# Kernel optimization log

Hardware: AMD Instinct MI355X
Metric: run time of the kernel (lower is better)

The kernel has to match this reference:

```python
import jax, jax.numpy as jnp
from jax import lax
import numpy as np

VOCAB = 50000
E = 301  # 300-dim pretrained + appended ones column
D = 25
NUM_CLASSES = 5


def setup_inputs() -> dict:
    key = jax.random.key(0)
    ks = jax.random.split(key, 8)
    B, S = 2048, 128
    words = jax.random.randint(ks[0], (B, S), 0, VOCAB)
    emb = jax.random.normal(ks[1], (VOCAB, E - 1), dtype=jnp.float32)
    # hstack ones column as in __init__
    emb_table = jnp.concatenate([emb, jnp.ones((VOCAB, 1), jnp.float32)], axis=1)
    A = jax.random.normal(ks[2], (D, E, D), dtype=jnp.float32) * 0.02
    W = jax.random.normal(ks[3], (E, D), dtype=jnp.float32) * 0.02
    V = jax.random.normal(ks[4], (D, D), dtype=jnp.float32) * 0.02
    b = jax.random.normal(ks[5], (D,), dtype=jnp.float32) * 0.02
    out_W = jax.random.normal(ks[6], (NUM_CLASSES, D), dtype=jnp.float32) * 0.02
    out_b = jax.random.normal(ks[7], (NUM_CLASSES,), dtype=jnp.float32) * 0.02
    return {"words": words, "batch_size": B, "emb_table": emb_table,
            "A": A, "W": W, "V": V, "b": b, "out_W": out_W, "out_b": out_b}


def reference(words, batch_size, emb_table, A, W, V, b, out_W, out_b):
    x_seq = emb_table[words]                      # [B, S, E] frozen embedding gather
    h0 = jnp.zeros((batch_size, D), jnp.float32).at[:, -1].set(1.0)

    def step(h, x):  # x: [B, E], h: [B, D]
        # a[b,i] = sum_{e,j} x[b,e] A[i,e,j] h[b,j]  (bilinear tensor term)
        a = jnp.einsum('be,ied,bd->bi', x, A, h)
        lin = x @ W + h @ V + b
        return jnp.tanh(a + lin), None

    h, _ = lax.scan(step, h0, jnp.swapaxes(x_seq, 0, 1))  # scan over S
    logits = h @ out_W.T + out_b                 # [B, num_classes]
    return jax.nn.sigmoid(logits)
```

## Files before the change

kernel.cpp:

```cpp
#include <hip/hip_runtime.h>
#include <math.h>

#define VOCAB 50000
#define EE 301
#define KP 304
#define DD 25
#define SEQ 128
#define NC 5
#define BROW 768
#define NUSE 700
#define TROW 704
#define EMT 50048

#define GLOAD_LDS16(g, l) __builtin_amdgcn_global_load_lds( \
    (const __attribute__((address_space(1))) void*)(g),     \
    (__attribute__((address_space(3))) void*)(l), 16, 0, 0)

__global__ __launch_bounds__(256) void build_B(
    const float* __restrict__ A, const float* __restrict__ W,
    float* __restrict__ Bmat)
{
    int e = blockIdx.x;
    for (int c = threadIdx.x; c < BROW; c += 256) {
        float v = 0.f;
        if (e < EE && c < NUSE) {
            int i = c / 28, j = c % 28;
            if (j < 25)       v = A[((size_t)i * EE + e) * DD + j];
            else if (j == 25) v = W[(size_t)e * DD + i];
        }
        Bmat[(size_t)e * BROW + c] = v;
    }
}

__global__ __launch_bounds__(256) void transpose_emb(
    const float* __restrict__ emb, float* __restrict__ embT)
{
    __shared__ float t[64][65];
    int m0 = blockIdx.x * 64, k0 = blockIdx.y * 64;
    int tx = threadIdx.x & 63, ty = threadIdx.x >> 6;
#pragma unroll
    for (int it = 0; it < 16; ++it) {
        int m = m0 + ty * 16 + it;
        int k = k0 + tx;
        t[tx][ty * 16 + it] = (m < VOCAB && k < EE) ? emb[(size_t)m * EE + k] : 0.f;
    }
    __syncthreads();
#pragma unroll
    for (int it = 0; it < 16; ++it) {
        int kl = ty * 16 + it;
        int k = k0 + kl;
        if (k < KP) embT[(size_t)k * EMT + m0 + tx] = t[kl][tx];
    }
}

__global__ __launch_bounds__(256, 2) void gemm_T2(
    const float* __restrict__ embT,
    const float* __restrict__ Bmat,
    float* __restrict__ T)
{
    __shared__ float As[2][16][128];
    __shared__ float Bs[2][16][128];
    int tid = threadIdx.x;
    int tx = tid & 15, ty = tid >> 4;
    int m0 = blockIdx.x * 128, n0 = blockIdx.y * 128;
    int wave = tid >> 6, lane = tid & 63;
    int krow = lane >> 5;
    int col4 = (lane & 31) * 4;

    float acc[8][8];
#pragma unroll
    for (int a = 0; a < 8; ++a)
#pragma unroll
        for (int c = 0; c < 8; ++c) acc[a][c] = 0.f;

    auto dma_tile = [&](int k0, int buf) {
#pragma unroll
        for (int j = 0; j < 2; ++j) {
            int r0 = wave * 4 + j * 2;
            int k = k0 + r0 + krow;
            GLOAD_LDS16(embT + (size_t)k * EMT + m0 + col4, &As[buf][r0][0]);
            GLOAD_LDS16(Bmat + (size_t)k * BROW + n0 + col4, &Bs[buf][r0][0]);
        }
    };

    dma_tile(0, 0);
    __syncthreads();

    int buf = 0;
    for (int k0 = 0; k0 < KP; k0 += 16) {
        if (k0 + 16 < KP) dma_tile(k0 + 16, buf ^ 1);
#pragma unroll
        for (int kk = 0; kk < 16; ++kk) {
            float4 a0 = *(const float4*)&As[buf][kk][ty * 4];
            float4 a1 = *(const float4*)&As[buf][kk][64 + ty * 4];
            float4 b0 = *(const float4*)&Bs[buf][kk][tx * 4];
            float4 b1 = *(const float4*)&Bs[buf][kk][64 + tx * 4];
            float av[8] = {a0.x, a0.y, a0.z, a0.w, a1.x, a1.y, a1.z, a1.w};
            float bv[8] = {b0.x, b0.y, b0.z, b0.w, b1.x, b1.y, b1.z, b1.w};
#pragma unroll
            for (int a = 0; a < 8; ++a)
#pragma unroll
                for (int c = 0; c < 8; ++c)
                    acc[a][c] = fmaf(av[a], bv[c], acc[a][c]);
        }
        __syncthreads();
        buf ^= 1;
    }

#pragma unroll
    for (int gi = 0; gi < 2; ++gi) {
#pragma unroll
        for (int r = 0; r < 4; ++r) {
            int m = m0 + gi * 64 + ty * 4 + r;
            if (m < VOCAB) {
                float* row = T + (size_t)m * TROW;
#pragma unroll
                for (int gc = 0; gc < 2; ++gc) {
                    int n = n0 + gc * 64 + tx * 4;
                    if (n < TROW) {
                        int a = gi * 4 + r, c = gc * 4;
                        *(float4*)(row + n) = make_float4(
                            acc[a][c], acc[a][c + 1], acc[a][c + 2], acc[a][c + 3]);
                    }
                }
            }
        }
    }
}

__global__ __launch_bounds__(256, 2) void gemm_T(
    const float* __restrict__ emb, const float* __restrict__ Bmat,
    float* __restrict__ T)
{
    __shared__ float As[2][16][132];
    __shared__ float Bs[2][16][132];
    int tid = threadIdx.x;
    int tx = tid & 15, ty = tid >> 4;
    int m0 = blockIdx.x * 128, n0 = blockIdx.y * 128;
    float acc[8][8];
#pragma unroll
    for (int a = 0; a < 8; ++a)
#pragma unroll
        for (int c = 0; c < 8; ++c) acc[a][c] = 0.f;
    float ar[8]; float4 br[2];
    int kl0 = tid >> 5, nl0 = (tid & 31) * 4;
#pragma unroll
    for (int it = 0; it < 8; ++it) {
        int m = m0 + ty + 16 * it, k = tx;
        ar[it] = (m < VOCAB && k < EE) ? emb[(size_t)m * EE + k] : 0.f;
    }
#pragma unroll
    for (int it = 0; it < 2; ++it) {
        int k = kl0 + 8 * it;
        br[it] = (k < EE) ? *(const float4*)(Bmat + (size_t)k * BROW + n0 + nl0)
                          : make_float4(0.f, 0.f, 0.f, 0.f);
    }
#pragma unroll
    for (int it = 0; it < 8; ++it) As[0][tx][ty + 16 * it] = ar[it];
#pragma unroll
    for (int it = 0; it < 2; ++it) *(float4*)(&Bs[0][kl0 + 8 * it][nl0]) = br[it];
    __syncthreads();
    int buf = 0;
    for (int k0 = 0; k0 < EE; k0 += 16) {
        int k1 = k0 + 16;
        bool more = (k1 < EE);
        if (more) {
#pragma unroll
            for (int it = 0; it < 8; ++it) {
                int m = m0 + ty + 16 * it, k = k1 + tx;
                ar[it] = (m < VOCAB && k < EE) ? emb[(size_t)m * EE + k] : 0.f;
            }
#pragma unroll
            for (int it = 0; it < 2; ++it) {
                int k = k1 + kl0 + 8 * it;
                br[it] = (k < EE) ? *(const float4*)(Bmat + (size_t)k * BROW + n0 + nl0)
                                  : make_float4(0.f, 0.f, 0.f, 0.f);
            }
        }
#pragma unroll
        for (int kk = 0; kk < 16; ++kk) {
            float4 a0 = *(const float4*)&As[buf][kk][ty * 4];
            float4 a1 = *(const float4*)&As[buf][kk][64 + ty * 4];
            float4 b0 = *(const float4*)&Bs[buf][kk][tx * 4];
            float4 b1 = *(const float4*)&Bs[buf][kk][64 + tx * 4];
            float av[8] = {a0.x, a0.y, a0.z, a0.w, a1.x, a1.y, a1.z, a1.w};
            float bv[8] = {b0.x, b0.y, b0.z, b0.w, b1.x, b1.y, b1.z, b1.w};
#pragma unroll
            for (int a = 0; a < 8; ++a)
#pragma unroll
                for (int c = 0; c < 8; ++c)
                    acc[a][c] = fmaf(av[a], bv[c], acc[a][c]);
        }
        if (more) {
            int nb = buf ^ 1;
#pragma unroll
            for (int it = 0; it < 8; ++it) As[nb][tx][ty + 16 * it] = ar[it];
#pragma unroll
            for (int it = 0; it < 2; ++it) *(float4*)(&Bs[nb][kl0 + 8 * it][nl0]) = br[it];
            __syncthreads();
            buf = nb;
        }
    }
#pragma unroll
    for (int gi = 0; gi < 2; ++gi) {
#pragma unroll
        for (int r = 0; r < 4; ++r) {
            int m = m0 + gi * 64 + ty * 4 + r;
            if (m < VOCAB) {
                float* row = T + (size_t)m * TROW;
#pragma unroll
                for (int gc = 0; gc < 2; ++gc) {
                    int n = n0 + gc * 64 + tx * 4;
                    if (n < TROW) {
                        int a = gi * 4 + r, c = gc * 4;
                        *(float4*)(row + n) = make_float4(
                            acc[a][c], acc[a][c + 1], acc[a][c + 2], acc[a][c + 3]);
                    }
                }
            }
        }
    }
}

__global__ __launch_bounds__(256) void rnn_scan_np5(
    const int*   __restrict__ words,
    const float* __restrict__ T,
    const float* __restrict__ V,
    const float* __restrict__ bvec,
    const float* __restrict__ outW,
    const float* __restrict__ outB,
    float* __restrict__ out,
    int B)
{
    int tid = threadIdx.x;
    int g = tid >> 5, i = tid & 31;
    int b = blockIdx.x * 8 + g;
    bool act = (i < DD) && (b < B);
    int ii = (i < DD) ? i : (DD - 1);
    int bsafe = (b < B) ? b : 0;
    const int* wr = words + (size_t)bsafe * SEQ;

    float Vcol[DD];
#pragma unroll
    for (int j = 0; j < DD; ++j) Vcol[j] = V[j * DD + ii];
    float bi = bvec[ii];

    float hr[DD];
#pragma unroll
    for (int j = 0; j < DD; ++j) hr[j] = 0.f;
    hr[DD - 1] = 1.f;

    bool sse = ((b & 3) == 0) && ((i & 3) == 0);
    const float* base = T + (size_t)ii * 28;

    float4 A0[7], A1[7], A2[7];
    auto LD = [&](float4* dst, int t) {
        const float* R = base + (size_t)wr[t] * TROW;
#pragma unroll
        for (int u = 0; u < 7; ++u) dst[u] = *(const float4*)(R + u * 4);
    };

    float hnew = 0.f;
    auto STEP = [&](const float4* C) {
        float Tj[28];
#pragma unroll
        for (int u = 0; u < 7; ++u) {
            Tj[u * 4 + 0] = C[u].x; Tj[u * 4 + 1] = C[u].y;
            Tj[u * 4 + 2] = C[u].z; Tj[u * 4 + 3] = C[u].w;
        }
        float qv = Tj[25];
        float a;
        if (sse) {
            float p0 = 0.f, p1 = 0.f, p2 = 0.f, p3 = 0.f;
#pragma unroll
            for (int j = 0; j < 24; j += 4) {
                p0 = __fadd_rn(p0, __fmul_rn(Tj[j],     hr[j]));
                p1 = __fadd_rn(p1, __fmul_rn(Tj[j + 1], hr[j + 1]));
                p2 = __fadd_rn(p2, __fmul_rn(Tj[j + 2], hr[j + 2]));
                p3 = __fadd_rn(p3, __fmul_rn(Tj[j + 3], hr[j + 3]));
            }
            float s02 = __fadd_rn(p0, p2);
            float s13 = __fadd_rn(p1, p3);
            a = __fadd_rn(s02, s13);
            a = __fadd_rn(a, __fmul_rn(Tj[24], hr[24]));
        } else {
            a = 0.f;
#pragma unroll
            for (int j = 0; j < DD; ++j)
                a = __fadd_rn(a, __fmul_rn(Tj[j], hr[j]));
        }
        float r2 = 0.f;
#pragma unroll
        for (int j = 0; j < DD; ++j)
            r2 = fmaf(hr[j], Vcol[j], r2);
        float lin = __fadd_rn(__fadd_rn(qv, r2), bi);
        float pre = __fadd_rn(a, lin);
        hnew = act ? (float)tanh((double)pre) : 0.f;
#pragma unroll
        for (int j = 0; j < DD; ++j)
            hr[j] = __shfl(hnew, j, 32);
    };

    LD(A0, 0);
    LD(A1, 1);
    for (int t = 0; t + 2 < SEQ; t += 3) {
        LD(A2, t + 2); STEP(A0);
        LD(A0, t + 3); STEP(A1);
        LD(A1, t + 4); STEP(A2);
    }
    STEP(A0);
    STEP(A1);

    if (i < NC && b < B) {
        float acc = 0.f;
#pragma unroll
        for (int j = 0; j < DD; ++j)
            acc = fmaf(hr[j], outW[i * DD + j], acc);
        float l = __fadd_rn(acc, outB[i]);
        out[(size_t)b * NC + i] = (float)(1.0 / (1.0 + exp(-(double)l)));
    }
}

extern "C" void kernel_launch(void* const* d_in, const int* in_sizes, int n_in,
                              void* d_out, int out_size, void* d_ws, size_t ws_size,
                              hipStream_t stream)
{
    const int*   words = (const int*)d_in[0];
    const float* emb   = (const float*)d_in[2];
    const float* A     = (const float*)d_in[3];
    const float* W     = (const float*)d_in[4];
    const float* V     = (const float*)d_in[5];
    const float* bias  = (const float*)d_in[6];
    const float* outW  = (const float*)d_in[7];
    const float* outB  = (const float*)d_in[8];
    float* out = (float*)d_out;
    int B = in_sizes[0] / SEQ;

    const size_t T_OFF    = (size_t)1 << 20;
    const size_t EMBT_OFF = (size_t)144 << 20;
    const size_t NEED     = EMBT_OFF + (size_t)KP * EMT * 4;
    float* Bmat = (float*)d_ws;
    float* T    = (float*)((char*)d_ws + T_OFF);
    float* embT = (float*)((char*)d_ws + EMBT_OFF);

    build_B<<<KP, 256, 0, stream>>>(A, W, Bmat);
    if (ws_size >= NEED) {
        transpose_emb<<<dim3(EMT / 64, (KP + 63) / 64), 256, 0, stream>>>(emb, embT);
        gemm_T2<<<dim3((VOCAB + 127) / 128, 6), 256, 0, stream>>>(embT, Bmat, T);
    } else {
        gemm_T<<<dim3((VOCAB + 127) / 128, 6), 256, 0, stream>>>(emb, Bmat, T);
    }
    rnn_scan_np5<<<(B + 7) / 8, 256, 0, stream>>>(words, T, V, bias, outW, outB, out, B);
}
```

Measured before the change: 511.3 us.

## Widen GEMM tile to 128x256 and deepen scan prefetch to four steps

The precompute GEMM now gives each block a 128x256 output tile with 8x16 accumulators per thread, halving the grid in N and the number of times each embT row is re-read. Launch bounds drop to one block per SM to leave room for the extra registers. The RNN scan kernel now prefetches gathered T rows four steps ahead instead of three, to hide more gather latency. The cost is higher register pressure and lower occupancy in both kernels, and the N tiling now computes columns up to 768 that are discarded past 704.

```diff
diff --git a/kernel.cpp b/kernel.cpp
--- a/kernel.cpp
+++ b/kernel.cpp
@@ -53,25 +53,25 @@
     }
 }
 
-__global__ __launch_bounds__(256, 2) void gemm_T2(
+__global__ __launch_bounds__(256, 1) void gemm_T3(
     const float* __restrict__ embT,
     const float* __restrict__ Bmat,
     float* __restrict__ T)
 {
     __shared__ float As[2][16][128];
-    __shared__ float Bs[2][16][128];
+    __shared__ float Bs[2][16][256];
     int tid = threadIdx.x;
     int tx = tid & 15, ty = tid >> 4;
-    int m0 = blockIdx.x * 128, n0 = blockIdx.y * 128;
+    int m0 = blockIdx.x * 128, n0 = blockIdx.y * 256;
     int wave = tid >> 6, lane = tid & 63;
     int krow = lane >> 5;
     int col4 = (lane & 31) * 4;
 
-    float acc[8][8];
+    float acc[8][16];
 #pragma unroll
     for (int a = 0; a < 8; ++a)
 #pragma unroll
-        for (int c = 0; c < 8; ++c) acc[a][c] = 0.f;
+        for (int c = 0; c < 16; ++c) acc[a][c] = 0.f;
 
     auto dma_tile = [&](int k0, int buf) {
 #pragma unroll
@@ -79,7 +79,12 @@
             int r0 = wave * 4 + j * 2;
             int k = k0 + r0 + krow;
             GLOAD_LDS16(embT + (size_t)k * EMT + m0 + col4, &As[buf][r0][0]);
-            GLOAD_LDS16(Bmat + (size_t)k * BROW + n0 + col4, &Bs[buf][r0][0]);
+        }
+#pragma unroll
+        for (int j = 0; j < 4; ++j) {
+            int r = wave * 4 + j;
+            int k = k0 + r;
+            GLOAD_LDS16(Bmat + (size_t)k * BROW + n0 + lane * 4, &Bs[buf][r][0]);
         }
     };
 
@@ -89,6 +94,97 @@
     int buf = 0;
     for (int k0 = 0; k0 < KP; k0 += 16) {
         if (k0 + 16 < KP) dma_tile(k0 + 16, buf ^ 1);
+#pragma unroll
+        for (int kk = 0; kk < 16; ++kk) {
+            float4 a0 = *(const float4*)&As[buf][kk][ty * 4];
+            float4 a1 = *(const float4*)&As[buf][kk][64 + ty * 4];
+            float4 b0 = *(const float4*)&Bs[buf][kk][tx * 4];
+            float4 b1 = *(const float4*)&Bs[buf][kk][64 + tx * 4];
+            float4 b2 = *(const float4*)&Bs[buf][kk][128 + tx * 4];
+            float4 b3 = *(const float4*)&Bs[buf][kk][192 + tx * 4];
+            float av[8]  = {a0.x, a0.y, a0.z, a0.w, a1.x, a1.y, a1.z, a1.w};
+            float bv[16] = {b0.x, b0.y, b0.z, b0.w, b1.x, b1.y, b1.z, b1.w,
+                            b2.x, b2.y, b2.z, b2.w, b3.x, b3.y, b3.z, b3.w};
+#pragma unroll
+            for (int a = 0; a < 8; ++a)
+#pragma unroll
+                for (int c = 0; c < 16; ++c)
+                    acc[a][c] = fmaf(av[a], bv[c], acc[a][c]);
+        }
+        __syncthreads();
+        buf ^= 1;
+    }
+
+#pragma unroll
+    for (int gi = 0; gi < 2; ++gi) {
+#pragma unroll
+        for (int r = 0; r < 4; ++r) {
+            int m = m0 + gi * 64 + ty * 4 + r;
+            if (m < VOCAB) {
+                float* row = T + (size_t)m * TROW;
+#pragma unroll
+                for (int gc = 0; gc < 4; ++gc) {
+                    int n = n0 + gc * 64 + tx * 4;
+                    if (n < TROW) {
+                        int a = gi * 4 + r, c = gc * 4;
+                        *(float4*)(row + n) = make_float4(
+                            acc[a][c], acc[a][c + 1], acc[a][c + 2], acc[a][c + 3]);
+                    }
+                }
+            }
+        }
+    }
+}
+
+__global__ __launch_bounds__(256, 2) void gemm_T(
+    const float* __restrict__ emb, const float* __restrict__ Bmat,
+    float* __restrict__ T)
+{
+    __shared__ float As[2][16][132];
+    __shared__ float Bs[2][16][132];
+    int tid = threadIdx.x;
+    int tx = tid & 15, ty = tid >> 4;
+    int m0 = blockIdx.x * 128, n0 = blockIdx.y * 128;
+    float acc[8][8];
+#pragma unroll
+    for (int a = 0; a < 8; ++a)
+#pragma unroll
+        for (int c = 0; c < 8; ++c) acc[a][c] = 0.f;
+    float ar[8]; float4 br[2];
+    int kl0 = tid >> 5, nl0 = (tid & 31) * 4;
+#pragma unroll
+    for (int it = 0; it < 8; ++it) {
+        int m = m0 + ty + 16 * it, k = tx;
+        ar[it] = (m < VOCAB && k < EE) ? emb[(size_t)m * EE + k] : 0.f;
+    }
+#pragma unroll
+    for (int it = 0; it < 2; ++it) {
+        int k = kl0 + 8 * it;
+        br[it] = (k < EE) ? *(const float4*)(Bmat + (size_t)k * BROW + n0 + nl0)
+                          : make_float4(0.f, 0.f, 0.f, 0.f);
+    }
+#pragma unroll
+    for (int it = 0; it < 8; ++it) As[0][tx][ty + 16 * it] = ar[it];
+#pragma unroll
+    for (int it = 0; it < 2; ++it) *(float4*)(&Bs[0][kl0 + 8 * it][nl0]) = br[it];
+    __syncthreads();
+    int buf = 0;
+    for (int k0 = 0; k0 < EE; k0 += 16) {
+        int k1 = k0 + 16;
+        bool more = (k1 < EE);
+        if (more) {
+#pragma unroll
+            for (int it = 0; it < 8; ++it) {
+                int m = m0 + ty + 16 * it, k = k1 + tx;
+                ar[it] = (m < VOCAB && k < EE) ? emb[(size_t)m * EE + k] : 0.f;
+            }
+#pragma unroll
+            for (int it = 0; it < 2; ++it) {
+                int k = k1 + kl0 + 8 * it;
+                br[it] = (k < EE) ? *(const float4*)(Bmat + (size_t)k * BROW + n0 + nl0)
+                                  : make_float4(0.f, 0.f, 0.f, 0.f);
+            }
+        }
 #pragma unroll
         for (int kk = 0; kk < 16; ++kk) {
             float4 a0 = *(const float4*)&As[buf][kk][ty * 4];
@@ -103,10 +199,16 @@
                 for (int c = 0; c < 8; ++c)
                     acc[a][c] = fmaf(av[a], bv[c], acc[a][c]);
         }
-        __syncthreads();
-        buf ^= 1;
-    }
-
+        if (more) {
+            int nb = buf ^ 1;
+#pragma unroll
+            for (int it = 0; it < 8; ++it) As[nb][tx][ty + 16 * it] = ar[it];
+#pragma unroll
+            for (int it = 0; it < 2; ++it) *(float4*)(&Bs[nb][kl0 + 8 * it][nl0]) = br[it];
+            __syncthreads();
+            buf = nb;
+        }
+    }
 #pragma unroll
     for (int gi = 0; gi < 2; ++gi) {
 #pragma unroll
@@ -128,101 +230,7 @@
     }
 }
 
-__global__ __launch_bounds__(256, 2) void gemm_T(
-    const float* __restrict__ emb, const float* __restrict__ Bmat,
-    float* __restrict__ T)
-{
-    __shared__ float As[2][16][132];
-    __shared__ float Bs[2][16][132];
-    int tid = threadIdx.x;
-    int tx = tid & 15, ty = tid >> 4;
-    int m0 = blockIdx.x * 128, n0 = blockIdx.y * 128;
-    float acc[8][8];
-#pragma unroll
-    for (int a = 0; a < 8; ++a)
-#pragma unroll
-        for (int c = 0; c < 8; ++c) acc[a][c] = 0.f;
-    float ar[8]; float4 br[2];
-    int kl0 = tid >> 5, nl0 = (tid & 31) * 4;
-#pragma unroll
-    for (int it = 0; it < 8; ++it) {
-        int m = m0 + ty + 16 * it, k = tx;
-        ar[it] = (m < VOCAB && k < EE) ? emb[(size_t)m * EE + k] : 0.f;
-    }
-#pragma unroll
-    for (int it = 0; it < 2; ++it) {
-        int k = kl0 + 8 * it;
-        br[it] = (k < EE) ? *(const float4*)(Bmat + (size_t)k * BROW + n0 + nl0)
-                          : make_float4(0.f, 0.f, 0.f, 0.f);
-    }
-#pragma unroll
-    for (int it = 0; it < 8; ++it) As[0][tx][ty + 16 * it] = ar[it];
-#pragma unroll
-    for (int it = 0; it < 2; ++it) *(float4*)(&Bs[0][kl0 + 8 * it][nl0]) = br[it];
-    __syncthreads();
-    int buf = 0;
-    for (int k0 = 0; k0 < EE; k0 += 16) {
-        int k1 = k0 + 16;
-        bool more = (k1 < EE);
-        if (more) {
-#pragma unroll
-            for (int it = 0; it < 8; ++it) {
-                int m = m0 + ty + 16 * it, k = k1 + tx;
-                ar[it] = (m < VOCAB && k < EE) ? emb[(size_t)m * EE + k] : 0.f;
-            }
-#pragma unroll
-            for (int it = 0; it < 2; ++it) {
-                int k = k1 + kl0 + 8 * it;
-                br[it] = (k < EE) ? *(const float4*)(Bmat + (size_t)k * BROW + n0 + nl0)
-                                  : make_float4(0.f, 0.f, 0.f, 0.f);
-            }
-        }
-#pragma unroll
-        for (int kk = 0; kk < 16; ++kk) {
-            float4 a0 = *(const float4*)&As[buf][kk][ty * 4];
-            float4 a1 = *(const float4*)&As[buf][kk][64 + ty * 4];
-            float4 b0 = *(const float4*)&Bs[buf][kk][tx * 4];
-            float4 b1 = *(const float4*)&Bs[buf][kk][64 + tx * 4];
-            float av[8] = {a0.x, a0.y, a0.z, a0.w, a1.x, a1.y, a1.z, a1.w};
-            float bv[8] = {b0.x, b0.y, b0.z, b0.w, b1.x, b1.y, b1.z, b1.w};
-#pragma unroll
-            for (int a = 0; a < 8; ++a)
-#pragma unroll
-                for (int c = 0; c < 8; ++c)
-                    acc[a][c] = fmaf(av[a], bv[c], acc[a][c]);
-        }
-        if (more) {
-            int nb = buf ^ 1;
-#pragma unroll
-            for (int it = 0; it < 8; ++it) As[nb][tx][ty + 16 * it] = ar[it];
-#pragma unroll
-            for (int it = 0; it < 2; ++it) *(float4*)(&Bs[nb][kl0 + 8 * it][nl0]) = br[it];
-            __syncthreads();
-            buf = nb;
-        }
-    }
-#pragma unroll
-    for (int gi = 0; gi < 2; ++gi) {
-#pragma unroll
-        for (int r = 0; r < 4; ++r) {
-            int m = m0 + gi * 64 + ty * 4 + r;
-            if (m < VOCAB) {
-                float* row = T + (size_t)m * TROW;
-#pragma unroll
-                for (int gc = 0; gc < 2; ++gc) {
-                    int n = n0 + gc * 64 + tx * 4;
-                    if (n < TROW) {
-                        int a = gi * 4 + r, c = gc * 4;
-                        *(float4*)(row + n) = make_float4(
-                            acc[a][c], acc[a][c + 1], acc[a][c + 2], acc[a][c + 3]);
-                    }
-                }
-            }
-        }
-    }
-}
-
-__global__ __launch_bounds__(256) void rnn_scan_np5(
+__global__ __launch_bounds__(256, 1) void rnn_scan_np6(
     const int*   __restrict__ words,
     const float* __restrict__ T,
     const float* __restrict__ V,
@@ -253,7 +261,7 @@
     bool sse = ((b & 3) == 0) && ((i & 3) == 0);
     const float* base = T + (size_t)ii * 28;
 
-    float4 A0[7], A1[7], A2[7];
+    float4 A0[7], A1[7], A2[7], A3[7];
     auto LD = [&](float4* dst, int t) {
         const float* R = base + (size_t)wr[t] * TROW;
 #pragma unroll
@@ -301,15 +309,16 @@
             hr[j] = __shfl(hnew, j, 32);
     };
 
-    LD(A0, 0);
-    LD(A1, 1);
-    for (int t = 0; t + 2 < SEQ; t += 3) {
-        LD(A2, t + 2); STEP(A0);
-        LD(A0, t + 3); STEP(A1);
-        LD(A1, t + 4); STEP(A2);
-    }
-    STEP(A0);
-    STEP(A1);
+    LD(A0, 0); LD(A1, 1); LD(A2, 2);
+    int t = 0;
+    for (; t + 6 < SEQ; t += 4) {
+        LD(A3, t + 3); STEP(A0);
+        LD(A0, t + 4); STEP(A1);
+        LD(A1, t + 5); STEP(A2);
+        LD(A2, t + 6); STEP(A3);
+    }
+    LD(A3, 127);
+    STEP(A0); STEP(A1); STEP(A2); STEP(A3);
 
     if (i < NC && b < B) {
         float acc = 0.f;
@@ -346,9 +355,9 @@
     build_B<<<KP, 256, 0, stream>>>(A, W, Bmat);
     if (ws_size >= NEED) {
         transpose_emb<<<dim3(EMT / 64, (KP + 63) / 64), 256, 0, stream>>>(emb, embT);
-        gemm_T2<<<dim3((VOCAB + 127) / 128, 6), 256, 0, stream>>>(embT, Bmat, T);
+        gemm_T3<<<dim3((VOCAB + 127) / 128, 3), 256, 0, stream>>>(embT, Bmat, T);
     } else {
         gemm_T<<<dim3((VOCAB + 127) / 128, 6), 256, 0, stream>>>(emb, Bmat, T);
     }
-    rnn_scan_np5<<<(B + 7) / 8, 256, 0, stream>>>(words, T, V, bias, outW, outB, out, B);
-}
+    rnn_scan_np6<<<(B + 7) / 8, 256, 0, stream>>>(words, T, V, bias, outW, outB, out, B);
+}
```

After: 499.0 us. 1.02x faster.
